# Kernel optimization log

Hardware: AMD Instinct MI355X
Metric: run time of the kernel (lower is better)

## Reference

```python
import jax, jax.numpy as jnp
import numpy as np
import math

D_MODEL, D_ENC, D_K, D_V, N_HEADS = 1024, 1024, 64, 64, 16
B, LQ, LK = 8, 1024, 1024


def setup_inputs() -> dict:
    key = jax.random.key(0)
    ks = jax.random.split(key, 9)
    # per-head Q/K/V linear params, stacked over heads (torch Linear: y = x @ W^T + b;
    # we store W already transposed as [in, out])
    lim_q = 1.0 / math.sqrt(D_MODEL)
    lim_e = 1.0 / math.sqrt(D_ENC)
    return {
        "decoder_batch": jax.random.normal(ks[0], (B, LQ, D_MODEL), jnp.float32),
        "encoder_out": jax.random.normal(ks[1], (B, LK, D_ENC), jnp.float32),
        "attn_mask": jax.random.randint(ks[2], (B, LQ, LK), 0, 2, jnp.int32),
        "Wq": jax.random.uniform(ks[3], (N_HEADS, D_MODEL, D_K), jnp.float32, -lim_q, lim_q),
        "bq": jax.random.uniform(ks[4], (N_HEADS, D_K), jnp.float32, -lim_q, lim_q),
        "Wk": jax.random.uniform(ks[5], (N_HEADS, D_ENC, D_K), jnp.float32, -lim_e, lim_e),
        "bk": jax.random.uniform(ks[6], (N_HEADS, D_K), jnp.float32, -lim_e, lim_e),
        "Wv": jax.random.uniform(ks[7], (N_HEADS, D_ENC, D_V), jnp.float32, -lim_e, lim_e),
        "bv": jax.random.uniform(ks[8], (N_HEADS, D_V), jnp.float32, -lim_e, lim_e),
    }


def reference(decoder_batch, encoder_out, attn_mask, Wq, bq, Wk, bk, Wv, bv):
    # Batched-over-heads version of the per-head Python loop (same math).
    q = jnp.einsum("bqd,hdk->bhqk", decoder_batch, Wq) + bq[None, :, None, :]
    k = jnp.einsum("bsd,hdk->bhsk", encoder_out, Wk) + bk[None, :, None, :]
    v = jnp.einsum("bsd,hdv->bhsv", encoder_out, Wv) + bv[None, :, None, :]
    scale = 1.0 / math.sqrt(D_K)
    logits = jnp.einsum("bhqk,bhsk->bhqs", q, k) * scale  # [B,H,LQ,LK]
    masked = attn_mask[:, None, :, :] == 0  # broadcast over heads
    # -inf mask; -1e30 yields exactly-zero probs for masked entries in fp32
    logits = jnp.where(masked, jnp.float32(-1e30), logits)
    scores = jax.nn.softmax(logits, axis=-1)
    # NaN fix: rows with all positions masked become all-zero (matches scores[scores!=scores]=0)
    all_masked = jnp.all(masked, axis=-1, keepdims=True)
    scores = jnp.where(all_masked, jnp.float32(0.0), scores)
    # dropout_prob=0.0 (eval) -> identity
    out = jnp.einsum("bhqs,bhsv->bhqv", scores, v)  # [B,H,LQ,D_V]
    # concat heads on last dim: [B,LQ,H*D_V]
    return out.transpose(0, 2, 1, 3).reshape(B, LQ, N_HEADS * D_V)
```

## Files before the change

kernel.cpp:

```cpp
#include <hip/hip_runtime.h>
#include <hip/hip_bf16.h>
#include <stdint.h>

#define DM   1024
#define DKV  64
#define NH   16
#define NB   8
#define SLEN 1024

typedef float  f32x4  __attribute__((ext_vector_type(4)));
typedef __bf16 bf16x8 __attribute__((ext_vector_type(8)));

#define L2E 1.44269504089f

__device__ __forceinline__ void gload_lds16(const void* g, void* l) {
  __builtin_amdgcn_global_load_lds(
      (const __attribute__((address_space(1))) void*)g,
      (__attribute__((address_space(3))) void*)l, 16, 0, 0);
}

__device__ __forceinline__ unsigned short f2bf(float f) {
  uint32_t u = __builtin_bit_cast(uint32_t, f);
  u += 0x7fffu + ((u >> 16) & 1u);
  return (unsigned short)(u >> 16);
}

__global__ void k_wT(const float* __restrict__ Wq, const float* __restrict__ Wk,
                     const float* __restrict__ Wv, unsigned short* __restrict__ Tq,
                     unsigned short* __restrict__ Tk, unsigned short* __restrict__ Tv) {
  __shared__ float tile[64][65];
  const int t = threadIdx.x;
  const int dc = blockIdx.x, h = blockIdx.y, s = blockIdx.z;
  const float* W = (s == 0) ? Wq : (s == 1) ? Wk : Wv;
  unsigned short* T = (s == 0) ? Tq : (s == 1) ? Tk : Tv;
#pragma unroll
  for (int i = 0; i < 4; ++i) {
    int idx = i * 256 + t;
    int d = idx >> 4, kg = idx & 15;
    float4 v = *(const float4*)(W + ((size_t)h * DM + dc * 64 + d) * DKV + kg * 4);
    tile[d][kg * 4 + 0] = v.x; tile[d][kg * 4 + 1] = v.y;
    tile[d][kg * 4 + 2] = v.z; tile[d][kg * 4 + 3] = v.w;
  }
  __syncthreads();
  int k = t >> 2, dg = t & 3;
  union { unsigned short u[8]; int4 v; } o0, o1;
#pragma unroll
  for (int j = 0; j < 8; ++j) o0.u[j] = f2bf(tile[dg * 16 + j][k]);
#pragma unroll
  for (int j = 0; j < 8; ++j) o1.u[j] = f2bf(tile[dg * 16 + 8 + j][k]);
  unsigned short* dst = T + ((size_t)h * DKV + k) * DM + dc * 64 + dg * 16;
  *(int4*)dst = o0.v;
  *(int4*)(dst + 8) = o1.v;
}

__global__ void k_pack(const int* __restrict__ m, uint32_t* __restrict__ out) {
  int wi = blockIdx.x * 256 + threadIdx.x;
  const int* p = m + (size_t)wi * 32;
  uint32_t bits = 0;
#pragma unroll
  for (int i = 0; i < 8; ++i) {
    int4 v = *(const int4*)(p + i * 4);
    bits |= ((uint32_t)(v.x != 0)) << (i * 4 + 0);
    bits |= ((uint32_t)(v.y != 0)) << (i * 4 + 1);
    bits |= ((uint32_t)(v.z != 0)) << (i * 4 + 2);
    bits |= ((uint32_t)(v.w != 0)) << (i * 4 + 3);
  }
  out[wi] = bits;
}

template <int EPI>
__global__ __launch_bounds__(256, 2)
void k_gemmF(const float* __restrict__ A, const unsigned short* __restrict__ BT,
             const float* __restrict__ bias, unsigned short* __restrict__ C) {
  __shared__ char As[8192];
  __shared__ char Bs[8192];
  const int t = threadIdx.x;
  const int w = t >> 6, lane = t & 63;
  const int g = lane >> 4, r16 = lane & 15;
  const int wm = w >> 1, wn = w & 1;
  const int m0 = blockIdx.y * 128, n0 = blockIdx.x * 128;
  const int arow = t >> 2, ac = t & 3;

  f32x4 acc[4][4] = {};
  for (int kt = 0; kt < DM / 32; ++kt) {
    float4 a0[2], a1[2];
#pragma unroll
    for (int i = 0; i < 2; ++i) {
      const float* src = A + (size_t)(m0 + arow + i * 64) * DM + kt * 32 + ac * 8;
      a0[i] = *(const float4*)src;
      a1[i] = *(const float4*)(src + 4);
    }
    __syncthreads();
#pragma unroll
    for (int i = 0; i < 2; ++i) {
      int row = arow + i * 64;
      int pos = ac ^ (row & 3);
      gload_lds16(BT + (size_t)(n0 + row) * DM + kt * 32 + pos * 8,
                  Bs + i * 4096 + w * 1024);
      union { unsigned short u[8]; int4 v; } o;
      o.u[0] = f2bf(a0[i].x); o.u[1] = f2bf(a0[i].y);
      o.u[2] = f2bf(a0[i].z); o.u[3] = f2bf(a0[i].w);
      o.u[4] = f2bf(a1[i].x); o.u[5] = f2bf(a1[i].y);
      o.u[6] = f2bf(a1[i].z); o.u[7] = f2bf(a1[i].w);
      *(int4*)(As + row * 64 + (pos << 4)) = o.v;
    }
    __syncthreads();
    bf16x8 af[4], bfr[4];
#pragma unroll
    for (int m = 0; m < 4; ++m) {
      int row = wm * 64 + m * 16 + r16;
      af[m] = *(const bf16x8*)(As + row * 64 + ((g ^ (row & 3)) << 4));
    }
#pragma unroll
    for (int n = 0; n < 4; ++n) {
      int row = wn * 64 + n * 16 + r16;
      bfr[n] = *(const bf16x8*)(Bs + row * 64 + ((g ^ (row & 3)) << 4));
    }
#pragma unroll
    for (int m = 0; m < 4; ++m)
#pragma unroll
      for (int n = 0; n < 4; ++n)
        acc[m][n] = __builtin_amdgcn_mfma_f32_16x16x32_bf16(af[m], bfr[n], acc[m][n], 0, 0, 0);
  }
#pragma unroll
  for (int m = 0; m < 4; ++m) {
    int rowb = m0 + wm * 64 + m * 16 + 4 * g;
#pragma unroll
    for (int n = 0; n < 4; ++n) {
      int col = n0 + wn * 64 + n * 16 + r16;
      float bv = bias[col];
      if (EPI == 0) {
#pragma unroll
        for (int r = 0; r < 4; ++r)
          C[(size_t)(rowb + r) * DM + col] = f2bf(acc[m][n][r] + bv);
      } else {
        int b = rowb >> 10, s = rowb & 1023;
        int h = col >> 6, v = col & 63;
        union { unsigned short u[4]; ushort4 q; } o;
#pragma unroll
        for (int r = 0; r < 4; ++r) o.u[r] = f2bf(acc[m][n][r] + bv);
        *(ushort4*)(C + (((size_t)(b * NH + h) * DKV + v) << 10) + s) = o.q;
      }
    }
  }
}

__global__ __launch_bounds__(256, 2)
void k_attn(const unsigned short* __restrict__ Q, const unsigned short* __restrict__ K,
            const unsigned short* __restrict__ VT, const uint32_t* __restrict__ MP,
            float* __restrict__ O) {
  __shared__ char Ks[8192];
  __shared__ char Vs[8192];
  __shared__ char Ps[8192];
  const int t = threadIdx.x, w = t >> 6, lane = t & 63;
  const int g = lane >> 4, r16 = lane & 15;
  const int qt = blockIdx.x, bh = blockIdx.y;
  const int b = bh >> 4, h = bh & 15;
  const int q0 = qt * 64 + w * 16;

  bf16x8 aq[2];
#pragma unroll
  for (int kc = 0; kc < 2; ++kc)
    aq[kc] = *(const bf16x8*)(Q + (size_t)(b * SLEN + q0 + r16) * DM + h * DKV + kc * 32 + g * 8);

  f32x4 oacc[4] = {};
  float mrun[4], lrun[4], anyv[4];
#pragma unroll
  for (int r = 0; r < 4; ++r) { mrun[r] = -1e30f; lrun[r] = 0.f; anyv[r] = 0.f; }

  const unsigned short* Kbase = K  + (size_t)b * SLEN * DM + h * DKV;
  const unsigned short* Vbase = VT + (size_t)bh * DKV * SLEN;
  const uint32_t*       Mbase = MP + (size_t)(b * SLEN + q0) * 32;

  for (int st = 0; st < 16; ++st) {
    const int s0 = st * 64;
    __syncthreads();
#pragma unroll
    for (int i = 0; i < 2; ++i) {
      int row  = (t >> 3) + i * 32;
      int slot = (t & 7) ^ (row & 7);
      gload_lds16(Kbase + (size_t)(s0 + row) * DM + slot * 8, Ks + i * 4096 + w * 1024);
      gload_lds16(Vbase + (size_t)row * SLEN + s0 + slot * 8, Vs + i * 4096 + w * 1024);
    }
    __syncthreads();

    f32x4 sacc[4];
#pragma unroll
    for (int f = 0; f < 4; ++f) {
      sacc[f] = (f32x4){0.f, 0.f, 0.f, 0.f};
#pragma unroll
      for (int kc = 0; kc < 2; ++kc) {
        int row = f * 16 + r16;
        int sl  = kc * 4 + g;
        bf16x8 bk_ = *(const bf16x8*)(Ks + row * 128 + ((sl ^ (row & 7)) << 4));
        sacc[f] = __builtin_amdgcn_mfma_f32_16x16x32_bf16(aq[kc], bk_, sacc[f], 0, 0, 0);
      }
    }

    uint32_t mw[4][2];
#pragma unroll
    for (int r = 0; r < 4; ++r)
#pragma unroll
      for (int fw = 0; fw < 2; ++fw)
        mw[r][fw] = Mbase[(size_t)(4 * g + r) * 32 + (s0 >> 5) + fw];

    float pv[4][4], mt[4];
#pragma unroll
    for (int r = 0; r < 4; ++r) mt[r] = -1e30f;
#pragma unroll
    for (int f = 0; f < 4; ++f) {
      uint32_t bit = 1u << (((f & 1) << 4) | r16);
#pragma unroll
      for (int r = 0; r < 4; ++r) {
        bool valid = (mw[r][f >> 1] & bit) != 0;
        float v = valid ? sacc[f][r] * 0.125f : -1e30f;
        pv[f][r] = v;
        mt[r] = fmaxf(mt[r], v);
      }
    }
#pragma unroll
    for (int d = 1; d < 16; d <<= 1)
#pragma unroll
      for (int r = 0; r < 4; ++r) mt[r] = fmaxf(mt[r], __shfl_xor(mt[r], d));

    float mnew[4], corr[4], lt[4];
#pragma unroll
    for (int r = 0; r < 4; ++r) {
      anyv[r] = fmaxf(anyv[r], (mt[r] > -5e29f) ? 1.f : 0.f);
      mnew[r] = fmaxf(mrun[r], mt[r]);
      corr[r] = exp2f((mrun[r] - mnew[r]) * L2E);
      lt[r] = 0.f;
    }
#pragma unroll
    for (int f = 0; f < 4; ++f)
#pragma unroll
      for (int r = 0; r < 4; ++r) {
        float p = exp2f((pv[f][r] - mnew[r]) * L2E);
        pv[f][r] = p;
        lt[r] += p;
      }
#pragma unroll
    for (int d = 1; d < 16; d <<= 1)
#pragma unroll
      for (int r = 0; r < 4; ++r) lt[r] += __shfl_xor(lt[r], d);
#pragma unroll
    for (int r = 0; r < 4; ++r) {
      lrun[r] = lrun[r] * corr[r] + lt[r];
      mrun[r] = mnew[r];
    }
#pragma unroll
    for (int n = 0; n < 4; ++n)
#pragma unroll
      for (int r = 0; r < 4; ++r) oacc[n][r] *= corr[r];

#pragma unroll
    for (int f = 0; f < 4; ++f)
#pragma unroll
      for (int r = 0; r < 4; ++r) {
        int qr = 4 * g + r;
        int col = f * 16 + r16;
        int byteoff = qr * 128 + (((col >> 3) ^ (qr & 7)) << 4) + ((col & 7) << 1);
        *(unsigned short*)(Ps + w * 2048 + byteoff) = f2bf(pv[f][r]);
      }

    bf16x8 pa[2];
#pragma unroll
    for (int ks = 0; ks < 2; ++ks) {
      int sl = ks * 4 + g;
      pa[ks] = *(const bf16x8*)(Ps + w * 2048 + r16 * 128 + ((sl ^ (r16 & 7)) << 4));
    }
#pragma unroll
    for (int n = 0; n < 4; ++n)
#pragma unroll
      for (int ks = 0; ks < 2; ++ks) {
        int row = n * 16 + r16;
        int sl  = ks * 4 + g;
        bf16x8 bv_ = *(const bf16x8*)(Vs + row * 128 + ((sl ^ (row & 7)) << 4));
        oacc[n] = __builtin_amdgcn_mfma_f32_16x16x32_bf16(pa[ks], bv_, oacc[n], 0, 0, 0);
      }
  }

  float inv[4];
#pragma unroll
  for (int r = 0; r < 4; ++r) inv[r] = (anyv[r] > 0.f) ? (1.f / lrun[r]) : 0.f;
#pragma unroll
  for (int n = 0; n < 4; ++n)
#pragma unroll
    for (int r = 0; r < 4; ++r)
      O[(size_t)(b * SLEN + q0 + 4 * g + r) * (NH * DKV) + h * DKV + n * 16 + r16] =
          oacc[n][r] * inv[r];
}

extern "C" void kernel_launch(void* const* d_in, const int* in_sizes, int n_in,
                              void* d_out, int out_size, void* d_ws, size_t ws_size,
                              hipStream_t stream) {
  const float* dec = (const float*)d_in[0];
  const float* enc = (const float*)d_in[1];
  const int*   msk = (const int*)d_in[2];
  const float* Wq  = (const float*)d_in[3];
  const float* bq  = (const float*)d_in[4];
  const float* Wk  = (const float*)d_in[5];
  const float* bk  = (const float*)d_in[6];
  const float* Wv  = (const float*)d_in[7];
  const float* bv  = (const float*)d_in[8];
  float* out = (float*)d_out;

  char* ws = (char*)d_ws;
  const size_t MB = 1ull << 20;
  unsigned short* Tq = (unsigned short*)(ws + 0);
  unsigned short* Tk = (unsigned short*)(ws + 2 * MB);
  unsigned short* Tv = (unsigned short*)(ws + 4 * MB);
  uint32_t*       MP = (uint32_t*)(ws + 6 * MB);
  unsigned short* Qb = (unsigned short*)(ws + 7 * MB);
  unsigned short* Kb = (unsigned short*)(ws + 23 * MB);
  unsigned short* VT = (unsigned short*)(ws + 39 * MB);

  k_wT<<<dim3(16, 16, 3), dim3(256), 0, stream>>>(Wq, Wk, Wv, Tq, Tk, Tv);
  k_pack<<<dim3(1024), dim3(256), 0, stream>>>(msk, MP);
  k_gemmF<0><<<dim3(8, 64), dim3(256), 0, stream>>>(dec, Tq, bq, Qb);
  k_gemmF<0><<<dim3(8, 64), dim3(256), 0, stream>>>(enc, Tk, bk, Kb);
  k_gemmF<1><<<dim3(8, 64), dim3(256), 0, stream>>>(enc, Tv, bv, VT);
  k_attn<<<dim3(16, 128), dim3(256), 0, stream>>>(Qb, Kb, VT, MP, out);
}
```

Baseline: 400.8 us.

## Transpose MFMA operands so each lane owns one query row in attention

Swaps the A/B operands of both MFMAs so the accumulator is transposed and each lane holds four key columns of a single query row. Row max and sum then need only two cross-lane shuffles instead of sixteen, and the running softmax state shrinks to one scalar per lane. The change also loads the mask with two words per lane, folds the scale and log2e into one multiply, uses the hardware exp2 and packed bf16 conversion, and writes P and the output as vector stores. Risks are a bf16 rounding mode that may differ from the old manual conversion and a slightly different rule for detecting fully masked rows.

```diff
diff --git a/kernel.cpp b/kernel.cpp
--- a/kernel.cpp
+++ b/kernel.cpp
@@ -157,23 +157,28 @@
   const int qt = blockIdx.x, bh = blockIdx.y;
   const int b = bh >> 4, h = bh & 15;
   const int q0 = qt * 64 + w * 16;
+  const int q = q0 + r16;
+  const int g4 = g * 4;
+  const int x7 = r16 & 7;
 
   bf16x8 aq[2];
 #pragma unroll
   for (int kc = 0; kc < 2; ++kc)
-    aq[kc] = *(const bf16x8*)(Q + (size_t)(b * SLEN + q0 + r16) * DM + h * DKV + kc * 32 + g * 8);
+    aq[kc] = *(const bf16x8*)(Q + (size_t)(b * SLEN + q) * DM + h * DKV + kc * 32 + g * 8);
 
   f32x4 oacc[4] = {};
-  float mrun[4], lrun[4], anyv[4];
-#pragma unroll
-  for (int r = 0; r < 4; ++r) { mrun[r] = -1e30f; lrun[r] = 0.f; anyv[r] = 0.f; }
+  float mrun = -1e30f, lrun = 0.f;
+  const float SCL = 0.125f * L2E;
 
   const unsigned short* Kbase = K  + (size_t)b * SLEN * DM + h * DKV;
   const unsigned short* Vbase = VT + (size_t)bh * DKV * SLEN;
-  const uint32_t*       Mbase = MP + (size_t)(b * SLEN + q0) * 32;
+  const uint32_t*       Mlane = MP + (size_t)(b * SLEN + q) * 32;
+  char* PsW = Ps + w * 2048 + r16 * 128;
 
   for (int st = 0; st < 16; ++st) {
     const int s0 = st * 64;
+    uint32_t mw0 = Mlane[(s0 >> 5) + 0] >> g4;
+    uint32_t mw1 = Mlane[(s0 >> 5) + 1] >> g4;
     __syncthreads();
 #pragma unroll
     for (int i = 0; i < 2; ++i) {
@@ -190,105 +195,79 @@
       sacc[f] = (f32x4){0.f, 0.f, 0.f, 0.f};
 #pragma unroll
       for (int kc = 0; kc < 2; ++kc) {
-        int row = f * 16 + r16;
-        int sl  = kc * 4 + g;
-        bf16x8 bk_ = *(const bf16x8*)(Ks + row * 128 + ((sl ^ (row & 7)) << 4));
-        sacc[f] = __builtin_amdgcn_mfma_f32_16x16x32_bf16(aq[kc], bk_, sacc[f], 0, 0, 0);
+        bf16x8 bk_ = *(const bf16x8*)(Ks + (f * 16 + r16) * 128 + (((kc * 4 + g) ^ x7) << 4));
+        sacc[f] = __builtin_amdgcn_mfma_f32_16x16x32_bf16(bk_, aq[kc], sacc[f], 0, 0, 0);
       }
     }
 
-    uint32_t mw[4][2];
-#pragma unroll
-    for (int r = 0; r < 4; ++r)
-#pragma unroll
-      for (int fw = 0; fw < 2; ++fw)
-        mw[r][fw] = Mbase[(size_t)(4 * g + r) * 32 + (s0 >> 5) + fw];
-
-    float pv[4][4], mt[4];
-#pragma unroll
-    for (int r = 0; r < 4; ++r) mt[r] = -1e30f;
 #pragma unroll
     for (int f = 0; f < 4; ++f) {
-      uint32_t bit = 1u << (((f & 1) << 4) | r16);
+      uint32_t mwf = (f < 2) ? mw0 : mw1;
 #pragma unroll
       for (int r = 0; r < 4; ++r) {
-        bool valid = (mw[r][f >> 1] & bit) != 0;
-        float v = valid ? sacc[f][r] * 0.125f : -1e30f;
-        pv[f][r] = v;
-        mt[r] = fmaxf(mt[r], v);
+        uint32_t bit = (mwf >> (((f & 1) << 4) + r)) & 1u;
+        sacc[f][r] = bit ? sacc[f][r] * SCL : -1e30f;
       }
     }
-#pragma unroll
-    for (int d = 1; d < 16; d <<= 1)
-#pragma unroll
-      for (int r = 0; r < 4; ++r) mt[r] = fmaxf(mt[r], __shfl_xor(mt[r], d));
-
-    float mnew[4], corr[4], lt[4];
-#pragma unroll
-    for (int r = 0; r < 4; ++r) {
-      anyv[r] = fmaxf(anyv[r], (mt[r] > -5e29f) ? 1.f : 0.f);
-      mnew[r] = fmaxf(mrun[r], mt[r]);
-      corr[r] = exp2f((mrun[r] - mnew[r]) * L2E);
-      lt[r] = 0.f;
-    }
+    float tm0 = fmaxf(fmaxf(sacc[0][0], sacc[0][1]), fmaxf(sacc[0][2], sacc[0][3]));
+    float tm1 = fmaxf(fmaxf(sacc[1][0], sacc[1][1]), fmaxf(sacc[1][2], sacc[1][3]));
+    float tm2 = fmaxf(fmaxf(sacc[2][0], sacc[2][1]), fmaxf(sacc[2][2], sacc[2][3]));
+    float tm3 = fmaxf(fmaxf(sacc[3][0], sacc[3][1]), fmaxf(sacc[3][2], sacc[3][3]));
+    float mt = fmaxf(fmaxf(tm0, tm1), fmaxf(tm2, tm3));
+    mt = fmaxf(mt, __shfl_xor(mt, 16));
+    mt = fmaxf(mt, __shfl_xor(mt, 32));
+
+    float mnew = fmaxf(mrun, mt);
+    float corr = __builtin_amdgcn_exp2f(mrun - mnew);
 #pragma unroll
     for (int f = 0; f < 4; ++f)
 #pragma unroll
-      for (int r = 0; r < 4; ++r) {
-        float p = exp2f((pv[f][r] - mnew[r]) * L2E);
-        pv[f][r] = p;
-        lt[r] += p;
+      for (int r = 0; r < 4; ++r)
+        sacc[f][r] = __builtin_amdgcn_exp2f(sacc[f][r] - mnew);
+    float ts0 = (sacc[0][0] + sacc[0][1]) + (sacc[0][2] + sacc[0][3]);
+    float ts1 = (sacc[1][0] + sacc[1][1]) + (sacc[1][2] + sacc[1][3]);
+    float ts2 = (sacc[2][0] + sacc[2][1]) + (sacc[2][2] + sacc[2][3]);
+    float ts3 = (sacc[3][0] + sacc[3][1]) + (sacc[3][2] + sacc[3][3]);
+    float lt = (ts0 + ts1) + (ts2 + ts3);
+    lt += __shfl_xor(lt, 16);
+    lt += __shfl_xor(lt, 32);
+    lrun = lrun * corr + lt;
+    mrun = mnew;
+#pragma unroll
+    for (int n = 0; n < 4; ++n) oacc[n] *= corr;
+
+#pragma unroll
+    for (int f = 0; f < 4; ++f) {
+      uint32_t lo, hi;
+      asm("v_cvt_pk_bf16_f32 %0, %1, %2" : "=v"(lo) : "v"(sacc[f][0]), "v"(sacc[f][1]));
+      asm("v_cvt_pk_bf16_f32 %0, %1, %2" : "=v"(hi) : "v"(sacc[f][2]), "v"(sacc[f][3]));
+      int slot = ((f << 2) | g) ^ (x7 << 1);
+      uint2 pk; pk.x = lo; pk.y = hi;
+      *(uint2*)(PsW + slot * 8) = pk;
+    }
+    bf16x8 pa[2];
+#pragma unroll
+    for (int kc = 0; kc < 2; ++kc)
+      pa[kc] = *(const bf16x8*)(PsW + (((kc * 4 + g) ^ x7) << 4));
+
+#pragma unroll
+    for (int n = 0; n < 4; ++n)
+#pragma unroll
+      for (int kc = 0; kc < 2; ++kc) {
+        bf16x8 bv_ = *(const bf16x8*)(Vs + (n * 16 + r16) * 128 + (((kc * 4 + g) ^ x7) << 4));
+        oacc[n] = __builtin_amdgcn_mfma_f32_16x16x32_bf16(bv_, pa[kc], oacc[n], 0, 0, 0);
       }
-#pragma unroll
-    for (int d = 1; d < 16; d <<= 1)
-#pragma unroll
-      for (int r = 0; r < 4; ++r) lt[r] += __shfl_xor(lt[r], d);
-#pragma unroll
-    for (int r = 0; r < 4; ++r) {
-      lrun[r] = lrun[r] * corr[r] + lt[r];
-      mrun[r] = mnew[r];
-    }
-#pragma unroll
-    for (int n = 0; n < 4; ++n)
-#pragma unroll
-      for (int r = 0; r < 4; ++r) oacc[n][r] *= corr[r];
-
-#pragma unroll
-    for (int f = 0; f < 4; ++f)
-#pragma unroll
-      for (int r = 0; r < 4; ++r) {
-        int qr = 4 * g + r;
-        int col = f * 16 + r16;
-        int byteoff = qr * 128 + (((col >> 3) ^ (qr & 7)) << 4) + ((col & 7) << 1);
-        *(unsigned short*)(Ps + w * 2048 + byteoff) = f2bf(pv[f][r]);
-      }
-
-    bf16x8 pa[2];
-#pragma unroll
-    for (int ks = 0; ks < 2; ++ks) {
-      int sl = ks * 4 + g;
-      pa[ks] = *(const bf16x8*)(Ps + w * 2048 + r16 * 128 + ((sl ^ (r16 & 7)) << 4));
-    }
-#pragma unroll
-    for (int n = 0; n < 4; ++n)
-#pragma unroll
-      for (int ks = 0; ks < 2; ++ks) {
-        int row = n * 16 + r16;
-        int sl  = ks * 4 + g;
-        bf16x8 bv_ = *(const bf16x8*)(Vs + row * 128 + ((sl ^ (row & 7)) << 4));
-        oacc[n] = __builtin_amdgcn_mfma_f32_16x16x32_bf16(pa[ks], bv_, oacc[n], 0, 0, 0);
-      }
-  }
-
-  float inv[4];
-#pragma unroll
-  for (int r = 0; r < 4; ++r) inv[r] = (anyv[r] > 0.f) ? (1.f / lrun[r]) : 0.f;
-#pragma unroll
-  for (int n = 0; n < 4; ++n)
-#pragma unroll
-    for (int r = 0; r < 4; ++r)
-      O[(size_t)(b * SLEN + q0 + 4 * g + r) * (NH * DKV) + h * DKV + n * 16 + r16] =
-          oacc[n][r] * inv[r];
+  }
+
+  float inv = (mrun > -5e29f) ? (1.f / lrun) : 0.f;
+  float* Orow = O + (size_t)(b * SLEN + q) * (NH * DKV) + h * DKV;
+#pragma unroll
+  for (int n = 0; n < 4; ++n) {
+    float4 o4;
+    o4.x = oacc[n][0] * inv; o4.y = oacc[n][1] * inv;
+    o4.z = oacc[n][2] * inv; o4.w = oacc[n][3] * inv;
+    *(float4*)(Orow + n * 16 + g4) = o4;
+  }
 }
 
 extern "C" void kernel_launch(void* const* d_in, const int* in_sizes, int n_in,
```

Measured after the change: 344.5 us. 1.16x faster.
